# Performance work log

Measured on AMD Instinct MI355X. Metric: run time of the kernel, lower is better.

## Reference

```python
import jax, jax.numpy as jnp
import numpy as np

N = 131072      # total points (divisible by patch size -> pad/unpad are identity)
C = 256         # channels
H = 8           # heads
K = 128         # patch size
HID = 1024      # mlp hidden (4*C)
SCALE = (C // H) ** -0.5
LN_EPS = 1e-5


def _ln(x, g, b):
    mu = jnp.mean(x, axis=-1, keepdims=True)
    var = jnp.mean((x - mu) ** 2, axis=-1, keepdims=True)
    return (x - mu) * jax.lax.rsqrt(var + LN_EPS) * g + b


def setup_inputs() -> dict:
    key = jax.random.key(0)
    ks = jax.random.split(key, 8)
    s = 0.02
    feat = jax.random.normal(ks[0], (N, C), jnp.float32)
    order = jax.random.permutation(ks[1], N)          # serialized order (padded)
    inverse = jnp.argsort(order)                      # unpad-composed inverse
    return {
        "feat": feat,
        "order": order.astype(jnp.int32),
        "inverse": inverse.astype(jnp.int32),
        "qkv_w": jax.random.normal(ks[2], (3 * C, C), jnp.float32) * s,
        "qkv_b": jnp.zeros((3 * C,), jnp.float32),
        "proj_w": jax.random.normal(ks[3], (C, C), jnp.float32) * s,
        "proj_b": jnp.zeros((C,), jnp.float32),
        "ln1_g": jnp.ones((C,), jnp.float32),
        "ln1_b": jnp.zeros((C,), jnp.float32),
        "ln2_g": jnp.ones((C,), jnp.float32),
        "ln2_b": jnp.zeros((C,), jnp.float32),
        "mlp_w1": jax.random.normal(ks[4], (HID, C), jnp.float32) * s,
        "mlp_b1": jnp.zeros((HID,), jnp.float32),
        "mlp_w2": jax.random.normal(ks[5], (C, HID), jnp.float32) * s,
        "mlp_b2": jnp.zeros((C,), jnp.float32),
    }


def reference(feat, order, inverse, qkv_w, qkv_b, proj_w, proj_b,
              ln1_g, ln1_b, ln2_g, ln2_b, mlp_w1, mlp_b1, mlp_w2, mlp_b2):
    d = C // H
    # --- pre-norm + serialized patch attention ---
    x = _ln(feat, ln1_g, ln1_b)
    qkv = x @ qkv_w.T + qkv_b                          # [N, 3C]
    qkv = qkv[order].reshape(N // K, K, 3, H, d)       # gather by serialized order
    q, k, v = qkv[:, :, 0], qkv[:, :, 1], qkv[:, :, 2] # [P, K, H, d]
    attn = jnp.einsum('pihd,pjhd->phij', q, k) * SCALE # per-patch scores
    attn = jax.nn.softmax(attn, axis=-1)
    out = jnp.einsum('phij,pjhd->pihd', attn, v).reshape(N, C)
    out = out[inverse]                                 # scatter back to point order
    out = out @ proj_w.T + proj_b
    x = feat + out                                     # residual
    # --- pre-norm MLP ---
    y = _ln(x, ln2_g, ln2_b)
    y = jax.nn.gelu(y @ mlp_w1.T + mlp_b1, approximate=False) @ mlp_w2.T + mlp_b2
    return x + y
```

## Files before the change

### kernel.cpp

```cpp
#include <hip/hip_runtime.h>

typedef unsigned short ushort;
typedef float f32x4 __attribute__((ext_vector_type(4)));
typedef __bf16 bf16x8 __attribute__((ext_vector_type(8)));

#define N_TOK 131072
#define C_DIM 256
#define H_HEADS 8
#define K_WIN 128
#define NB (N_TOK / K_WIN)
#define ATTN_SCALE 0.17677669529663687f
#define LN_EPS 1e-5f

__device__ __forceinline__ ushort f2b(float f) {
  unsigned u = __float_as_uint(f);
  unsigned r = (u + 0x7fffu + ((u >> 16) & 1u)) >> 16;
  return (ushort)r;
}

__device__ __forceinline__ void cp16(const void* gptr, void* lptr) {
  __builtin_amdgcn_global_load_lds(
      (const __attribute__((address_space(1))) unsigned int*)(unsigned long long)gptr,
      (__attribute__((address_space(3))) unsigned int*)(unsigned)(unsigned long long)lptr,
      16, 0, 0);
}

__global__ void f2b_kernel(const float* __restrict__ in, ushort* __restrict__ out, int n) {
  int i = blockIdx.x * 256 + threadIdx.x;
  if (i < n) out[i] = f2b(in[i]);
}

__global__ __launch_bounds__(256) void ln_kernel(const float* __restrict__ x,
                                                 const float* __restrict__ g,
                                                 const float* __restrict__ b,
                                                 ushort* __restrict__ out) {
  int row = blockIdx.x * 4 + (threadIdx.x >> 6);
  int lane = threadIdx.x & 63;
  const float4* px = reinterpret_cast<const float4*>(x + (size_t)row * C_DIM);
  float4 v = px[lane];
  float s = v.x + v.y + v.z + v.w;
#pragma unroll
  for (int off = 32; off; off >>= 1) s += __shfl_xor(s, off);
  float mu = s * (1.0f / C_DIM);
  float dx = v.x - mu, dy = v.y - mu, dz = v.z - mu, dw = v.w - mu;
  float q = dx * dx + dy * dy + dz * dz + dw * dw;
#pragma unroll
  for (int off = 32; off; off >>= 1) q += __shfl_xor(q, off);
  float rstd = rsqrtf(q * (1.0f / C_DIM) + LN_EPS);
  float4 gv = reinterpret_cast<const float4*>(g)[lane];
  float4 bv = reinterpret_cast<const float4*>(b)[lane];
  ushort4 o;
  o.x = f2b(dx * rstd * gv.x + bv.x);
  o.y = f2b(dy * rstd * gv.y + bv.y);
  o.z = f2b(dz * rstd * gv.z + bv.z);
  o.w = f2b(dw * rstd * gv.w + bv.w);
  reinterpret_cast<ushort4*>(out + (size_t)row * C_DIM)[lane] = o;
}

template <int EPI>
__global__ __launch_bounds__(256, 2) void gemm_bt(
    const ushort* __restrict__ A, const ushort* __restrict__ B,
    const float* __restrict__ bias, void* __restrict__ out,
    const int* __restrict__ scatter, const float* __restrict__ resid,
    int M, int Nn, int Kk) {
  __shared__ ushort sA[128 * 32];
  __shared__ ushort sB[128 * 32];
  const int tid = threadIdx.x;
  const int wave = tid >> 6;
  const int lane = tid & 63;
  const int quad = lane >> 4;
  const int l16 = lane & 15;
  const int ntn = Nn >> 7;
  const int mt = blockIdx.x / ntn;
  const int nt = blockIdx.x % ntn;
  const int m0 = mt << 7, n0 = nt << 7;
  const int rw = (wave >> 1) << 6;
  const int cw = (wave & 1) << 6;
  const int c0 = tid, c1 = tid + 256;

  f32x4 acc[4][4] = {};

  for (int k0 = 0; k0 < Kk; k0 += 32) {
    __syncthreads();
    cp16(A + ((size_t)(m0 + (c0 >> 2)) * Kk + k0 + (c0 & 3) * 8), sA + wave * 512);
    cp16(A + ((size_t)(m0 + (c1 >> 2)) * Kk + k0 + (c1 & 3) * 8), sA + 2048 + wave * 512);
    cp16(B + ((size_t)(n0 + (c0 >> 2)) * Kk + k0 + (c0 & 3) * 8), sB + wave * 512);
    cp16(B + ((size_t)(n0 + (c1 >> 2)) * Kk + k0 + (c1 & 3) * 8), sB + 2048 + wave * 512);
    __syncthreads();

    bf16x8 af[4], bfr[4];
#pragma unroll
    for (int i = 0; i < 4; i++)
      af[i] = *(const bf16x8*)(sA + (rw + i * 16 + l16) * 32 + quad * 8);
#pragma unroll
    for (int i = 0; i < 4; i++)
      bfr[i] = *(const bf16x8*)(sB + (cw + i * 16 + l16) * 32 + quad * 8);
#pragma unroll
    for (int mi = 0; mi < 4; mi++)
#pragma unroll
      for (int ni = 0; ni < 4; ni++)
        acc[mi][ni] = __builtin_amdgcn_mfma_f32_16x16x32_bf16(af[mi], bfr[ni], acc[mi][ni], 0, 0, 0);
  }

  float bv[4];
#pragma unroll
  for (int ni = 0; ni < 4; ni++) bv[ni] = bias[n0 + cw + ni * 16 + l16];

#pragma unroll
  for (int mi = 0; mi < 4; mi++) {
#pragma unroll
    for (int r = 0; r < 4; r++) {
      int row = m0 + rw + mi * 16 + quad * 4 + r;
      if (EPI == 0) {
        int orow = scatter[row];
        ushort* po = (ushort*)out + (size_t)orow * Nn + n0 + cw + l16;
#pragma unroll
        for (int ni = 0; ni < 4; ni++) po[ni * 16] = f2b(acc[mi][ni][r] + bv[ni]);
      } else if (EPI == 1) {
        size_t base = (size_t)row * Nn + n0 + cw + l16;
        float* po = (float*)out;
#pragma unroll
        for (int ni = 0; ni < 4; ni++)
          po[base + ni * 16] = acc[mi][ni][r] + bv[ni] + resid[base + ni * 16];
      } else {
        ushort* po = (ushort*)out + (size_t)row * Nn + n0 + cw + l16;
#pragma unroll
        for (int ni = 0; ni < 4; ni++) {
          float v = acc[mi][ni][r] + bv[ni];
          po[ni * 16] = f2b(0.5f * v * (1.0f + erff(v * 0.70710678f)));
        }
      }
    }
  }
}

__global__ __launch_bounds__(256, 2) void attn_kernel(
    const ushort* __restrict__ qkv, const int* __restrict__ order,
    ushort* __restrict__ out) {
  __shared__ ushort sQ[128 * 32];
  __shared__ ushort sK[128 * 32];
  __shared__ ushort sVt[32 * 136];
  __shared__ ushort sP[128 * 136];
  const int p = blockIdx.x >> 3;
  const int h = blockIdx.x & 7;
  const int tid = threadIdx.x;
  const int wave = tid >> 6, lane = tid & 63;
  const int quad = lane >> 4, l16 = lane & 15;
  const size_t rowbase = (size_t)(p * K_WIN) * 768;

  {
    int a = tid, b = tid + 256;
    const ushort* gq0 = qkv + rowbase + (size_t)(a >> 2) * 768 + h * 32 + (a & 3) * 8;
    const ushort* gq1 = qkv + rowbase + (size_t)(b >> 2) * 768 + h * 32 + (b & 3) * 8;
    cp16(gq0, sQ + wave * 512);
    cp16(gq1, sQ + 2048 + wave * 512);
    cp16(gq0 + 256, sK + wave * 512);
    cp16(gq1 + 256, sK + 2048 + wave * 512);
  }
  {
    int r = tid >> 1, cb = (tid & 1) * 16;
    const ushort* gv = qkv + rowbase + (size_t)r * 768 + 512 + h * 32 + cb;
    __align__(16) ushort tmp[16];
    *(uint4*)(tmp) = *(const uint4*)(gv);
    *(uint4*)(tmp + 8) = *(const uint4*)(gv + 8);
#pragma unroll
    for (int i = 0; i < 16; i++) sVt[(cb + i) * 136 + r] = tmp[i];
  }
  __syncthreads();

  const int rw2 = wave * 32;
  f32x4 s[2][8] = {};
  bf16x8 qa[2];
#pragma unroll
  for (int mi = 0; mi < 2; mi++)
    qa[mi] = *(const bf16x8*)(sQ + (rw2 + mi * 16 + l16) * 32 + quad * 8);
#pragma unroll
  for (int nj = 0; nj < 8; nj++) {
    bf16x8 kb = *(const bf16x8*)(sK + (nj * 16 + l16) * 32 + quad * 8);
#pragma unroll
    for (int mi = 0; mi < 2; mi++)
      s[mi][nj] = __builtin_amdgcn_mfma_f32_16x16x32_bf16(qa[mi], kb, s[mi][nj], 0, 0, 0);
  }

#pragma unroll
  for (int mi = 0; mi < 2; mi++) {
#pragma unroll
    for (int r = 0; r < 4; r++) {
      float t[8];
      float mx = -1e30f;
#pragma unroll
      for (int nj = 0; nj < 8; nj++) {
        t[nj] = s[mi][nj][r] * ATTN_SCALE;
        mx = fmaxf(mx, t[nj]);
      }
#pragma unroll
      for (int off = 1; off < 16; off <<= 1) mx = fmaxf(mx, __shfl_xor(mx, off));
      float sm = 0.0f;
#pragma unroll
      for (int nj = 0; nj < 8; nj++) {
        t[nj] = __expf(t[nj] - mx);
        sm += t[nj];
      }
#pragma unroll
      for (int off = 1; off < 16; off <<= 1) sm += __shfl_xor(sm, off);
      float inv = 1.0f / sm;
      int prow = rw2 + mi * 16 + quad * 4 + r;
#pragma unroll
      for (int nj = 0; nj < 8; nj++)
        sP[prow * 136 + nj * 16 + l16] = f2b(t[nj] * inv);
    }
  }
  __syncthreads();

  f32x4 o[2][2] = {};
#pragma unroll
  for (int kk = 0; kk < 4; kk++) {
    bf16x8 pa[2], vb[2];
#pragma unroll
    for (int mi = 0; mi < 2; mi++)
      pa[mi] = *(const bf16x8*)(sP + (rw2 + mi * 16 + l16) * 136 + kk * 32 + quad * 8);
#pragma unroll
    for (int ni = 0; ni < 2; ni++)
      vb[ni] = *(const bf16x8*)(sVt + (ni * 16 + l16) * 136 + kk * 32 + quad * 8);
#pragma unroll
    for (int mi = 0; mi < 2; mi++)
#pragma unroll
      for (int ni = 0; ni < 2; ni++)
        o[mi][ni] = __builtin_amdgcn_mfma_f32_16x16x32_bf16(pa[mi], vb[ni], o[mi][ni], 0, 0, 0);
  }

#pragma unroll
  for (int mi = 0; mi < 2; mi++) {
#pragma unroll
    for (int r = 0; r < 4; r++) {
      int row = rw2 + mi * 16 + quad * 4 + r;
      int g = order[p * K_WIN + row];
      ushort* po = out + (size_t)g * C_DIM + h * 32 + l16;
      po[0] = f2b(o[mi][0][r]);
      po[16] = f2b(o[mi][1][r]);
    }
  }
}

extern "C" void kernel_launch(void* const* d_in, const int* in_sizes, int n_in,
                              void* d_out, int out_size, void* d_ws, size_t ws_size,
                              hipStream_t stream) {
  const float* feat = (const float*)d_in[0];
  const int* order = (const int*)d_in[1];
  const int* inverse = (const int*)d_in[2];
  const float* qkv_w = (const float*)d_in[3];
  const float* qkv_b = (const float*)d_in[4];
  const float* proj_w = (const float*)d_in[5];
  const float* proj_b = (const float*)d_in[6];
  const float* ln1_g = (const float*)d_in[7];
  const float* ln1_b = (const float*)d_in[8];
  const float* ln2_g = (const float*)d_in[9];
  const float* ln2_b = (const float*)d_in[10];
  const float* mlp_w1 = (const float*)d_in[11];
  const float* mlp_b1 = (const float*)d_in[12];
  const float* mlp_w2 = (const float*)d_in[13];
  const float* mlp_b2 = (const float*)d_in[14];
  float* out = (float*)d_out;

  char* ws = (char*)d_ws;
  ushort* xln = (ushort*)(ws);
  ushort* qkvp = (ushort*)(ws + 67108864);
  ushort* attn = (ushort*)(ws + 67108864 + 201326592);
  ushort* hbuf = qkvp;
  ushort* wq = (ushort*)(ws + 335544320);
  ushort* wp = wq + 196608;
  ushort* w1 = wp + 65536;
  ushort* w2 = w1 + 262144;

  f2b_kernel<<<768, 256, 0, stream>>>(qkv_w, wq, 196608);
  f2b_kernel<<<256, 256, 0, stream>>>(proj_w, wp, 65536);
  f2b_kernel<<<1024, 256, 0, stream>>>(mlp_w1, w1, 262144);
  f2b_kernel<<<1024, 256, 0, stream>>>(mlp_w2, w2, 262144);

  ln_kernel<<<N_TOK / 4, 256, 0, stream>>>(feat, ln1_g, ln1_b, xln);
  gemm_bt<0><<<(N_TOK / 128) * 6, 256, 0, stream>>>(xln, wq, qkv_b, qkvp, inverse, nullptr,
                                                    N_TOK, 768, 256);
  attn_kernel<<<NB * H_HEADS, 256, 0, stream>>>(qkvp, order, attn);
  gemm_bt<1><<<(N_TOK / 128) * 2, 256, 0, stream>>>(attn, wp, proj_b, out, nullptr, feat,
                                                    N_TOK, 256, 256);
  ln_kernel<<<N_TOK / 4, 256, 0, stream>>>(out, ln2_g, ln2_b, xln);
  gemm_bt<2><<<(N_TOK / 128) * 8, 256, 0, stream>>>(xln, w1, mlp_b1, hbuf, nullptr, nullptr,
                                                    N_TOK, 1024, 256);
  gemm_bt<1><<<(N_TOK / 128) * 2, 256, 0, stream>>>(hbuf, w2, mlp_b2, out, nullptr, out,
                                                    N_TOK, 256, 1024);
}
```

Measured before the change: 868.2 us.

## Deepen GEMM K-tile with swizzled LDS, XCD-aware block mapping, gather qkv in attention

The GEMM K step grows from 32 to 64, and an XOR swizzle on the LDS layout is meant to avoid bank conflicts, halving the number of barrier pairs per tile. Blocks are remapped so that consecutive M tiles land on the same XCD, for better L2 reuse of A and B. The QKV GEMM now writes rows in point order, and the attention kernel gathers rows through order[] instead of the GEMM scattering through inverse[]. This trades a contiguous GEMM store for a gathered attention load, and doubles LDS use per block.

Result: faster. 826.3 us (-4.8%).

```diff
diff --git a/kernel.cpp b/kernel.cpp
--- a/kernel.cpp
+++ b/kernel.cpp
@@ -61,45 +61,57 @@
 __global__ __launch_bounds__(256, 2) void gemm_bt(
     const ushort* __restrict__ A, const ushort* __restrict__ B,
     const float* __restrict__ bias, void* __restrict__ out,
-    const int* __restrict__ scatter, const float* __restrict__ resid,
-    int M, int Nn, int Kk) {
-  __shared__ ushort sA[128 * 32];
-  __shared__ ushort sB[128 * 32];
+    const float* __restrict__ resid, int M, int Nn, int Kk) {
+  __shared__ ushort sA[128 * 64];
+  __shared__ ushort sB[128 * 64];
   const int tid = threadIdx.x;
   const int wave = tid >> 6;
   const int lane = tid & 63;
   const int quad = lane >> 4;
   const int l16 = lane & 15;
   const int ntn = Nn >> 7;
-  const int mt = blockIdx.x / ntn;
-  const int nt = blockIdx.x % ntn;
+  const int nmt = M >> 7;
+  const int x = blockIdx.x & 7;
+  const int i = blockIdx.x >> 3;
+  const int mt = x * (nmt >> 3) + i / ntn;
+  const int nt = i % ntn;
   const int m0 = mt << 7, n0 = nt << 7;
   const int rw = (wave >> 1) << 6;
   const int cw = (wave & 1) << 6;
-  const int c0 = tid, c1 = tid + 256;
+  const int lrow = lane >> 3;
+  const int sch = ((lane & 7) ^ lrow) << 3;
 
   f32x4 acc[4][4] = {};
 
-  for (int k0 = 0; k0 < Kk; k0 += 32) {
+  for (int k0 = 0; k0 < Kk; k0 += 64) {
     __syncthreads();
-    cp16(A + ((size_t)(m0 + (c0 >> 2)) * Kk + k0 + (c0 & 3) * 8), sA + wave * 512);
-    cp16(A + ((size_t)(m0 + (c1 >> 2)) * Kk + k0 + (c1 & 3) * 8), sA + 2048 + wave * 512);
-    cp16(B + ((size_t)(n0 + (c0 >> 2)) * Kk + k0 + (c0 & 3) * 8), sB + wave * 512);
-    cp16(B + ((size_t)(n0 + (c1 >> 2)) * Kk + k0 + (c1 & 3) * 8), sB + 2048 + wave * 512);
+#pragma unroll
+    for (int j = 0; j < 4; j++) {
+      int r = (wave << 5) + (j << 3) + lrow;
+      cp16(A + ((size_t)(m0 + r) * Kk + k0 + sch), sA + (wave << 11) + (j << 9));
+      cp16(B + ((size_t)(n0 + r) * Kk + k0 + sch), sB + (wave << 11) + (j << 9));
+    }
     __syncthreads();
 
-    bf16x8 af[4], bfr[4];
-#pragma unroll
-    for (int i = 0; i < 4; i++)
-      af[i] = *(const bf16x8*)(sA + (rw + i * 16 + l16) * 32 + quad * 8);
-#pragma unroll
-    for (int i = 0; i < 4; i++)
-      bfr[i] = *(const bf16x8*)(sB + (cw + i * 16 + l16) * 32 + quad * 8);
-#pragma unroll
-    for (int mi = 0; mi < 4; mi++)
-#pragma unroll
-      for (int ni = 0; ni < 4; ni++)
-        acc[mi][ni] = __builtin_amdgcn_mfma_f32_16x16x32_bf16(af[mi], bfr[ni], acc[mi][ni], 0, 0, 0);
+#pragma unroll
+    for (int kk = 0; kk < 2; kk++) {
+      bf16x8 af[4], bfr[4];
+#pragma unroll
+      for (int ii = 0; ii < 4; ii++) {
+        int row = rw + ii * 16 + l16;
+        af[ii] = *(const bf16x8*)(sA + row * 64 + ((((kk << 2) | quad) ^ (row & 7)) << 3));
+      }
+#pragma unroll
+      for (int ii = 0; ii < 4; ii++) {
+        int row = cw + ii * 16 + l16;
+        bfr[ii] = *(const bf16x8*)(sB + row * 64 + ((((kk << 2) | quad) ^ (row & 7)) << 3));
+      }
+#pragma unroll
+      for (int mi = 0; mi < 4; mi++)
+#pragma unroll
+        for (int ni = 0; ni < 4; ni++)
+          acc[mi][ni] = __builtin_amdgcn_mfma_f32_16x16x32_bf16(af[mi], bfr[ni], acc[mi][ni], 0, 0, 0);
+    }
   }
 
   float bv[4];
@@ -112,8 +124,7 @@
     for (int r = 0; r < 4; r++) {
       int row = m0 + rw + mi * 16 + quad * 4 + r;
       if (EPI == 0) {
-        int orow = scatter[row];
-        ushort* po = (ushort*)out + (size_t)orow * Nn + n0 + cw + l16;
+        ushort* po = (ushort*)out + (size_t)row * Nn + n0 + cw + l16;
 #pragma unroll
         for (int ni = 0; ni < 4; ni++) po[ni * 16] = f2b(acc[mi][ni][r] + bv[ni]);
       } else if (EPI == 1) {
@@ -141,17 +152,20 @@
   __shared__ ushort sK[128 * 32];
   __shared__ ushort sVt[32 * 136];
   __shared__ ushort sP[128 * 136];
-  const int p = blockIdx.x >> 3;
-  const int h = blockIdx.x & 7;
+  const int xcd = blockIdx.x & 7;
+  const int bi = blockIdx.x >> 3;
+  const int p = (bi >> 3) * 8 + xcd;
+  const int h = bi & 7;
   const int tid = threadIdx.x;
   const int wave = tid >> 6, lane = tid & 63;
   const int quad = lane >> 4, l16 = lane & 15;
-  const size_t rowbase = (size_t)(p * K_WIN) * 768;
 
   {
     int a = tid, b = tid + 256;
-    const ushort* gq0 = qkv + rowbase + (size_t)(a >> 2) * 768 + h * 32 + (a & 3) * 8;
-    const ushort* gq1 = qkv + rowbase + (size_t)(b >> 2) * 768 + h * 32 + (b & 3) * 8;
+    int ga = order[p * K_WIN + (a >> 2)];
+    int gb = order[p * K_WIN + (b >> 2)];
+    const ushort* gq0 = qkv + (size_t)ga * 768 + h * 32 + (a & 3) * 8;
+    const ushort* gq1 = qkv + (size_t)gb * 768 + h * 32 + (b & 3) * 8;
     cp16(gq0, sQ + wave * 512);
     cp16(gq1, sQ + 2048 + wave * 512);
     cp16(gq0 + 256, sK + wave * 512);
@@ -159,7 +173,8 @@
   }
   {
     int r = tid >> 1, cb = (tid & 1) * 16;
-    const ushort* gv = qkv + rowbase + (size_t)r * 768 + 512 + h * 32 + cb;
+    int gr = order[p * K_WIN + r];
+    const ushort* gv = qkv + (size_t)gr * 768 + 512 + h * 32 + cb;
     __align__(16) ushort tmp[16];
     *(uint4*)(tmp) = *(const uint4*)(gv);
     *(uint4*)(tmp + 8) = *(const uint4*)(gv + 8);
@@ -247,7 +262,6 @@
                               hipStream_t stream) {
   const float* feat = (const float*)d_in[0];
   const int* order = (const int*)d_in[1];
-  const int* inverse = (const int*)d_in[2];
   const float* qkv_w = (const float*)d_in[3];
   const float* qkv_b = (const float*)d_in[4];
   const float* proj_w = (const float*)d_in[5];
@@ -278,14 +292,14 @@
   f2b_kernel<<<1024, 256, 0, stream>>>(mlp_w2, w2, 262144);
 
   ln_kernel<<<N_TOK / 4, 256, 0, stream>>>(feat, ln1_g, ln1_b, xln);
-  gemm_bt<0><<<(N_TOK / 128) * 6, 256, 0, stream>>>(xln, wq, qkv_b, qkvp, inverse, nullptr,
+  gemm_bt<0><<<(N_TOK / 128) * 6, 256, 0, stream>>>(xln, wq, qkv_b, qkvp, nullptr,
                                                     N_TOK, 768, 256);
   attn_kernel<<<NB * H_HEADS, 256, 0, stream>>>(qkvp, order, attn);
-  gemm_bt<1><<<(N_TOK / 128) * 2, 256, 0, stream>>>(attn, wp, proj_b, out, nullptr, feat,
+  gemm_bt<1><<<(N_TOK / 128) * 2, 256, 0, stream>>>(attn, wp, proj_b, out, feat,
                                                     N_TOK, 256, 256);
   ln_kernel<<<N_TOK / 4, 256, 0, stream>>>(out, ln2_g, ln2_b, xln);
-  gemm_bt<2><<<(N_TOK / 128) * 8, 256, 0, stream>>>(xln, w1, mlp_b1, hbuf, nullptr, nullptr,
+  gemm_bt<2><<<(N_TOK / 128) * 8, 256, 0, stream>>>(xln, w1, mlp_b1, hbuf, nullptr,
                                                     N_TOK, 1024, 256);
-  gemm_bt<1><<<(N_TOK / 128) * 2, 256, 0, stream>>>(hbuf, w2, mlp_b2, out, nullptr, out,
+  gemm_bt<1><<<(N_TOK / 128) * 2, 256, 0, stream>>>(hbuf, w2, mlp_b2, out, out,
                                                     N_TOK, 256, 1024);
 }
```
